# Optimization experiments

Measured on AMD Instinct MI355X. Metric: run time of the kernel, lower is better.

## Reference

```python
import jax, jax.numpy as jnp
import numpy as np

B, S, D, H, HS, OUT = 2, 2048, 1024, 16, 64, 1024
NEG = 1e12


def setup_inputs() -> dict:
    key = jax.random.key(0)
    ks = jax.random.split(key, 12)
    def glorot(k, shape):
        lim = np.sqrt(6.0 / (shape[0] + shape[1]))
        return jax.random.uniform(k, shape, jnp.float32, -lim, lim)
    return {
        'query': jax.random.normal(ks[0], (B, S, D), jnp.float32),
        'key':   jax.random.normal(ks[1], (B, S, D), jnp.float32),
        'value': jax.random.normal(ks[2], (B, S, D), jnp.float32),
        'Wq': glorot(ks[3], (D, H * HS)), 'bq': jnp.zeros((H * HS,), jnp.float32),
        'Wk': glorot(ks[4], (D, H * HS)), 'bk': jnp.zeros((H * HS,), jnp.float32),
        'Wv': glorot(ks[5], (D, H * HS)), 'bv': jnp.zeros((H * HS,), jnp.float32),
        'Wo': glorot(ks[6], (H * HS, OUT)), 'bo': jnp.zeros((OUT,), jnp.float32),
        'q_mask': jax.random.randint(ks[7], (B, S), 0, 2, jnp.int32),
        'v_mask': jax.random.randint(ks[8], (B, S), 0, 2, jnp.int32),
    }


def reference(query, key, value, Wq, bq, Wk, bk, Wv, bv, Wo, bo, q_mask, v_mask):
    qm = q_mask.astype(query.dtype)  # [B,Sq]
    vm = v_mask.astype(query.dtype)  # [B,Sk]
    # projections -> [B,S,H,HS]
    q = (query @ Wq + bq).reshape(B, S, H, HS)
    k = (key @ Wk + bk).reshape(B, S, H, HS)
    v = (value @ Wv + bv).reshape(B, S, H, HS)
    # scores [B,H,Sq,Sk]; code always divides by sqrt(head_size)
    a = jnp.einsum('bqhd,bkhd->bhqk', q, k) / np.sqrt(HS).astype(np.float32)
    a = a - (1.0 - vm[:, None, None, :]) * NEG  # additive padding mask on keys
    a = jax.nn.softmax(a, axis=-1)
    o = jnp.einsum('bhqk,bkhd->bqhd', a, v).reshape(B, S, H * HS)
    o = o @ Wo + bo
    o = o * qm[:, :, None]  # zero out padded query positions
    return o
```

## Files before the change

kernel.cpp:

```cpp
#include <hip/hip_runtime.h>

#define Bz 2
#define Sz 2048
#define Dz 1024
#define Hz 16
#define HSz 64
#define Mz 4096
#define NEGB (-1e30f)
#define CEXP 12.0f
#define QSCALE (0.125f * 1.44269504088896f)

typedef _Float16 f16;
typedef _Float16 f16x8 __attribute__((ext_vector_type(8)));
typedef _Float16 f16x4 __attribute__((ext_vector_type(4)));
typedef float f32x4 __attribute__((ext_vector_type(4)));

#define MFMA32(a, b, c) __builtin_amdgcn_mfma_f32_16x16x32_f16((a), (b), (c), 0, 0, 0)
#define MFMA16(a, b, c) __builtin_amdgcn_mfma_f32_16x16x16f16((a), (b), (c), 0, 0, 0)
#define EXP2(x) __builtin_amdgcn_exp2f(x)

__device__ __forceinline__ void gload16(const void* g, void* l) {
  __builtin_amdgcn_global_load_lds(
      (const __attribute__((address_space(1))) unsigned int*)(unsigned long long)g,
      (__attribute__((address_space(3))) unsigned int*)(unsigned int)(unsigned long long)l,
      16, 0, 0);
}
__device__ __forceinline__ void gload4(const void* g, void* l) {
  __builtin_amdgcn_global_load_lds(
      (const __attribute__((address_space(1))) unsigned int*)(unsigned long long)g,
      (__attribute__((address_space(3))) unsigned int*)(unsigned int)(unsigned long long)l,
      4, 0, 0);
}

__global__ __launch_bounds__(256) void k_prep(
    const float* __restrict__ q, const float* __restrict__ k,
    const float* __restrict__ v, f16* __restrict__ oq, f16* __restrict__ ok,
    f16* __restrict__ ov, const float* __restrict__ W0,
    const float* __restrict__ W1, const float* __restrict__ W2,
    const float* __restrict__ W3, f16* __restrict__ T0, f16* __restrict__ T1,
    f16* __restrict__ T2, f16* __restrict__ T3, const int* __restrict__ vm,
    float* __restrict__ vmb) {
  __shared__ float tbuf[32][33];
  const int bid = blockIdx.x;
  if (bid < 12288) {
    const int s = bid >> 12, cb = bid & 4095;
    const float* in = s == 0 ? q : s == 1 ? k : v;
    f16* out = s == 0 ? oq : s == 1 ? ok : ov;
    int i = (cb * 256 + threadIdx.x) * 4;
    f32x4 vv = *reinterpret_cast<const f32x4*>(in + i);
    f16x4 o;
    o[0] = (f16)vv[0]; o[1] = (f16)vv[1]; o[2] = (f16)vv[2]; o[3] = (f16)vv[3];
    *reinterpret_cast<f16x4*>(out + i) = o;
  } else if (bid < 16384) {
    const int r = bid - 12288;
    const int z = r >> 10, xy = r & 1023;
    const float* W = z == 0 ? W0 : z == 1 ? W1 : z == 2 ? W2 : W3;
    f16* T = z == 0 ? T0 : z == 1 ? T1 : z == 2 ? T2 : T3;
    const int tx = threadIdx.x & 31, ty = threadIdx.x >> 5;
    const int n0 = (xy & 31) * 32, k0 = (xy >> 5) * 32;
#pragma unroll
    for (int rr = 0; rr < 4; ++rr)
      tbuf[ty * 4 + rr][tx] = W[(size_t)(k0 + ty * 4 + rr) * Dz + n0 + tx];
    __syncthreads();
#pragma unroll
    for (int rr = 0; rr < 4; ++rr)
      T[(size_t)(n0 + ty * 4 + rr) * Dz + k0 + tx] = (f16)tbuf[tx][ty * 4 + rr];
  } else {
    int i = (bid - 16384) * 256 + threadIdx.x;
    vmb[i] = vm[i] ? -CEXP : NEGB;
  }
}

#define BMg 128
#define BNg 128
#define BKg 64
#define NKT (Dz / BKg)

#define GEMM_MAINLOOP(Aptr, Bptr)                                              \
  f32x4 acc[4][2] = {};                                                        \
  auto stage = [&](int kt, int buf) {                                          \
    const int k0 = kt * BKg;                                                   \
    _Pragma("unroll") for (int j = 0; j < 2; ++j) {                            \
      int c = j * 512 + t;                                                     \
      int row = c >> 3, p = c & 7;                                             \
      int ke = (p ^ (row & 7)) * 8;                                            \
      gload16(Aptr + (size_t)(m0 + row) * Dz + k0 + ke,                        \
              (char*)&As[buf][0] + c * 16);                                    \
      gload16(Bptr + (size_t)(n0 + row) * Dz + k0 + ke,                        \
              (char*)&Bs[buf][0] + c * 16);                                    \
    }                                                                          \
  };                                                                           \
  stage(0, 0);                                                                 \
  __syncthreads();                                                             \
  for (int kt = 0; kt < NKT; ++kt) {                                           \
    const int cur = kt & 1;                                                    \
    if (kt + 1 < NKT) stage(kt + 1, cur ^ 1);                                  \
    __builtin_amdgcn_s_setprio(1);                                             \
    _Pragma("unroll") for (int ks = 0; ks < 2; ++ks) {                         \
      f16x8 af[4], bf[2];                                                      \
      _Pragma("unroll") for (int fr = 0; fr < 4; ++fr) {                       \
        const int row = wr * 64 + fr * 16 + ll;                                \
        af[fr] = *reinterpret_cast<const f16x8*>(                              \
            &As[cur][row * 64 + (((ks * 4 + lh) ^ (row & 7)) * 8)]);           \
      }                                                                        \
      _Pragma("unroll") for (int fc = 0; fc < 2; ++fc) {                       \
        const int col = wc * 32 + fc * 16 + ll;                                \
        bf[fc] = *reinterpret_cast<const f16x8*>(                              \
            &Bs[cur][col * 64 + (((ks * 4 + lh) ^ (col & 7)) * 8)]);           \
      }                                                                        \
      _Pragma("unroll") for (int fr = 0; fr < 4; ++fr)                         \
          _Pragma("unroll") for (int fc = 0; fc < 2; ++fc)                     \
              acc[fr][fc] = MFMA32(af[fr], bf[fc], acc[fr][fc]);               \
    }                                                                          \
    __builtin_amdgcn_s_setprio(0);                                             \
    __syncthreads();                                                           \
  }

__global__ __launch_bounds__(512) void k_gemm_qkv(
    const f16* __restrict__ Xq, const f16* __restrict__ Xk,
    const f16* __restrict__ Xv, const f16* __restrict__ Wq,
    const f16* __restrict__ Wk, const f16* __restrict__ Wv,
    const float* __restrict__ bq, const float* __restrict__ bk,
    const float* __restrict__ bv, f16* __restrict__ Qh, f16* __restrict__ Kh,
    f16* __restrict__ Vth) {
  __shared__ f16 As[2][BMg * BKg];
  __shared__ f16 Bs[2][BNg * BKg];
  const int z = blockIdx.z;
  const f16* A = z == 0 ? Xq : z == 1 ? Xk : Xv;
  const f16* Bt = z == 0 ? Wq : z == 1 ? Wk : Wv;
  const float* bias = z == 0 ? bq : z == 1 ? bk : bv;
  f16* outh = z == 0 ? Qh : z == 1 ? Kh : Vth;
  const float oscale = z == 0 ? QSCALE : 1.0f;
  const int t = threadIdx.x, lane = t & 63, wv = t >> 6;
  const int ll = lane & 15, lh = lane >> 4;
  const int m0 = blockIdx.y * BMg, n0 = blockIdx.x * BNg;
  const int wr = wv >> 2, wc = wv & 3;

  GEMM_MAINLOOP(A, Bt)

#pragma unroll
  for (int fc = 0; fc < 2; ++fc) {
    const int n = n0 + wc * 32 + fc * 16 + ll;
    const float bn = bias[n];
#pragma unroll
    for (int fr = 0; fr < 4; ++fr)
#pragma unroll
      for (int i = 0; i < 4; ++i) {
        const int m = m0 + wr * 64 + fr * 16 + lh * 4 + i;
        float v = (acc[fr][fc][i] + bn) * oscale;
        if (z < 2) {
          outh[((size_t)((m >> 11) * Hz + (n >> 6))) * (Sz * HSz) +
               (size_t)(m & (Sz - 1)) * HSz + (n & 63)] = (f16)v;
        } else {
          outh[((size_t)((m >> 11) * Hz + (n >> 6))) * (HSz * Sz) +
               (size_t)(n & 63) * Sz + (m & (Sz - 1))] = (f16)v;
        }
      }
  }
}

__global__ __launch_bounds__(512) void k_gemm_o(
    const f16* __restrict__ A, const f16* __restrict__ Bt,
    const float* __restrict__ bias, float* __restrict__ outf,
    const int* __restrict__ qmask) {
  __shared__ f16 As[2][BMg * BKg];
  __shared__ f16 Bs[2][BNg * BKg];
  const int t = threadIdx.x, lane = t & 63, wv = t >> 6;
  const int ll = lane & 15, lh = lane >> 4;
  const int m0 = blockIdx.y * BMg, n0 = blockIdx.x * BNg;
  const int wr = wv >> 2, wc = wv & 3;

  GEMM_MAINLOOP(A, Bt)

#pragma unroll
  for (int fc = 0; fc < 2; ++fc) {
    const int n = n0 + wc * 32 + fc * 16 + ll;
    const float bn = bias[n];
#pragma unroll
    for (int fr = 0; fr < 4; ++fr)
#pragma unroll
      for (int i = 0; i < 4; ++i) {
        const int m = m0 + wr * 64 + fr * 16 + lh * 4 + i;
        outf[(size_t)m * Dz + n] = (acc[fr][fc][i] + bn) * (float)qmask[m];
      }
  }
}

#define QB 128
#define KBc 64
#define NST (Sz / (2 * KBc))

__global__ __launch_bounds__(256, 4) void k_attn(
    const f16* __restrict__ Q, const f16* __restrict__ K,
    const f16* __restrict__ Vt, const float* __restrict__ vmb,
    f16* __restrict__ attnA) {
  __shared__ f16 Kl[4][KBc * 64];
  __shared__ f16 Vl[4][HSz * 64];
  __shared__ float mbl[4][KBc];
  const int t = threadIdx.x, lane = t & 63, wv = t >> 6;
  const int ll = lane & 15, lh = lane >> 4;
  const int bh = blockIdx.y, b = bh >> 4, h = bh & 15;
  const int q0 = blockIdx.x * QB + wv * 32;
  const size_t base = (size_t)bh * Sz * HSz;

  f16x8 qf[2][2];
#pragma unroll
  for (int qs = 0; qs < 2; ++qs) {
    const f16* Qb = Q + base + (size_t)(q0 + qs * 16 + ll) * HSz;
    qf[qs][0] = *reinterpret_cast<const f16x8*>(&Qb[lh * 8]);
    qf[qs][1] = *reinterpret_cast<const f16x8*>(&Qb[32 + lh * 8]);
  }

  f32x4 acc0[4] = {}, acc1[4] = {};
  f32x4 accl0 = {}, accl1 = {};
  const f16x4 vone = {(f16)1.f, (f16)1.f, (f16)1.f, (f16)1.f};

  auto stage = [&](int key0, int pair) {
#pragma unroll
    for (int sb = 0; sb < 2; ++sb) {
      const int bi = pair * 2 + sb;
#pragma unroll
      for (int j = 0; j < 2; ++j) {
        int c = j * 256 + t;
        int r = c >> 3, p = c & 7, ps = (p ^ (r & 7)) * 8;
        gload16(K + base + (size_t)(key0 + sb * KBc + r) * HSz + ps,
                (char*)&Kl[bi][0] + c * 16);
        gload16(Vt + base + (size_t)r * Sz + key0 + sb * KBc + ps,
                (char*)&Vl[bi][0] + c * 16);
      }
      if (wv == 0)
        gload4(vmb + b * Sz + key0 + sb * KBc + lane,
               (char*)&mbl[bi][0] + lane * 4);
    }
  };

  auto tile = [&](int bi) {
    f32x4 sa0[4], sa1[4];
#pragma unroll
    for (int cf = 0; cf < 4; ++cf) {
      f32x4 mb = *reinterpret_cast<const f32x4*>(&mbl[bi][cf * 16 + lh * 4]);
      sa0[cf] = mb;
      sa1[cf] = mb;
    }
    __builtin_amdgcn_s_setprio(1);
#pragma unroll
    for (int cf = 0; cf < 4; ++cf) {
      const int row = cf * 16 + ll;
      const f16* kr = &Kl[bi][row * 64];
      f16x8 ka0 = *reinterpret_cast<const f16x8*>(&kr[(lh ^ (ll & 7)) * 8]);
      f16x8 ka1 = *reinterpret_cast<const f16x8*>(&kr[((4 + lh) ^ (ll & 7)) * 8]);
      sa0[cf] = MFMA32(ka0, qf[0][0], sa0[cf]);
      sa0[cf] = MFMA32(ka1, qf[0][1], sa0[cf]);
      sa1[cf] = MFMA32(ka0, qf[1][0], sa1[cf]);
      sa1[cf] = MFMA32(ka1, qf[1][1], sa1[cf]);
    }
    __builtin_amdgcn_s_setprio(0);

    f16x4 pb0[4], pb1[4];
#pragma unroll
    for (int cf = 0; cf < 4; ++cf) {
#pragma unroll
      for (int i = 0; i < 4; ++i) {
        pb0[cf][i] = (f16)EXP2(sa0[cf][i]);
        pb1[cf][i] = (f16)EXP2(sa1[cf][i]);
      }
    }

    __builtin_amdgcn_s_setprio(1);
#pragma unroll
    for (int hf = 0; hf < 4; ++hf) {
      const int row = hf * 16 + ll;
      const f16* vr = &Vl[bi][row * 64];
#pragma unroll
      for (int cf = 0; cf < 4; ++cf) {
        f16x4 va = *reinterpret_cast<const f16x4*>(
            &vr[((2 * cf + (lh >> 1)) ^ (ll & 7)) * 8 + (lh & 1) * 4]);
        acc0[hf] = MFMA16(va, pb0[cf], acc0[hf]);
        acc1[hf] = MFMA16(va, pb1[cf], acc1[hf]);
      }
    }
#pragma unroll
    for (int cf = 0; cf < 4; ++cf) {
      accl0 = MFMA16(vone, pb0[cf], accl0);
      accl1 = MFMA16(vone, pb1[cf], accl1);
    }
    __builtin_amdgcn_s_setprio(0);
  };

  stage(0, 0);
  __syncthreads();

  for (int st = 0; st < NST; ++st) {
    const int cur = st & 1;
    if (st + 1 < NST) stage((st + 1) * 2 * KBc, cur ^ 1);
    tile(cur * 2);
    tile(cur * 2 + 1);
    __syncthreads();
  }

#pragma unroll
  for (int qs = 0; qs < 2; ++qs) {
    const float l_run = qs ? accl1[0] : accl0[0];
    const float inv = 1.f / fmaxf(l_run, 1e-37f);
    const int q = q0 + qs * 16 + ll;
    f16* orow = attnA + (size_t)(b * Sz + q) * (Hz * HSz) + h * HSz;
#pragma unroll
    for (int hf = 0; hf < 4; ++hf) {
      const f32x4& a = qs ? acc1[hf] : acc0[hf];
      f16x4 ov;
#pragma unroll
      for (int i = 0; i < 4; ++i) ov[i] = (f16)(a[i] * inv);
      *reinterpret_cast<f16x4*>(&orow[hf * 16 + 4 * lh]) = ov;
    }
  }
}

extern "C" void kernel_launch(void* const* d_in, const int* in_sizes, int n_in,
                              void* d_out, int out_size, void* d_ws, size_t ws_size,
                              hipStream_t stream) {
  const float* query = (const float*)d_in[0];
  const float* key   = (const float*)d_in[1];
  const float* value = (const float*)d_in[2];
  const float* Wq = (const float*)d_in[3];
  const float* bq = (const float*)d_in[4];
  const float* Wk = (const float*)d_in[5];
  const float* bk = (const float*)d_in[6];
  const float* Wv = (const float*)d_in[7];
  const float* bv = (const float*)d_in[8];
  const float* Wo = (const float*)d_in[9];
  const float* bo = (const float*)d_in[10];
  const int* qm = (const int*)d_in[11];
  const int* vm = (const int*)d_in[12];

  f16* Xq  = (f16*)d_ws;
  f16* Xk  = Xq + 4194304;
  f16* Xv  = Xk + 4194304;
  f16* Wqh = Xv + 4194304;
  f16* Wkh = Wqh + 1048576;
  f16* Wvh = Wkh + 1048576;
  f16* Woh = Wvh + 1048576;
  f16* Qh  = Woh + 1048576;
  f16* Kh  = Qh + 4194304;
  f16* Vth = Kh + 4194304;
  f16* Ah  = Vth + 4194304;
  float* vmbias = (float*)(Ah + 4194304);

  k_prep<<<16400, 256, 0, stream>>>(query, key, value, Xq, Xk, Xv, Wq, Wk, Wv,
                                    Wo, Wqh, Wkh, Wvh, Woh, vm, vmbias);

  dim3 gq(Dz / BNg, Mz / BMg, 3);
  k_gemm_qkv<<<gq, 512, 0, stream>>>(Xq, Xk, Xv, Wqh, Wkh, Wvh, bq, bk, bv,
                                     Qh, Kh, Vth);

  dim3 ag(Sz / QB, Bz * Hz);
  k_attn<<<ag, 256, 0, stream>>>(Qh, Kh, Vth, vmbias, Ah);

  dim3 gg(Dz / BNg, Mz / BMg);
  k_gemm_o<<<gg, 512, 0, stream>>>(Ah, Woh, bo, (float*)d_out, qm);
}
```

Before: 130.9 us.

## Permute V-transpose key order for 16-byte LDS reads; shrink attention staging to 64-key tiles

The V projection epilogue now writes keys in a permuted order within each 64-key block, so the attention kernel can read V fragments as one 16-byte LDS load per pair of MFMA16 steps instead of two 8-byte loads. The permutation is consistent because P columns and V rows share the same permuted key order, and the sum over keys is unaffected. The attention loop is also restructured from 2×64-key stages over 4 LDS buffers to single 64-key tiles over 2 buffers. This halves LDS use, which could raise occupancy, but adds twice as many barriers per key sweep.

```diff
diff --git a/kernel.cpp b/kernel.cpp
--- a/kernel.cpp
+++ b/kernel.cpp
@@ -152,8 +152,9 @@
           outh[((size_t)((m >> 11) * Hz + (n >> 6))) * (Sz * HSz) +
                (size_t)(m & (Sz - 1)) * HSz + (n & 63)] = (f16)v;
         } else {
+          const int mp = (m & ~63) | (32 * (fr >> 1) + 8 * lh + 4 * (fr & 1) + i);
           outh[((size_t)((m >> 11) * Hz + (n >> 6))) * (HSz * Sz) +
-               (size_t)(n & 63) * Sz + (m & (Sz - 1))] = (f16)v;
+               (size_t)(n & 63) * Sz + (mp & (Sz - 1))] = (f16)v;
         }
       }
   }
@@ -188,15 +189,15 @@
 
 #define QB 128
 #define KBc 64
-#define NST (Sz / (2 * KBc))
+#define NT (Sz / KBc)
 
 __global__ __launch_bounds__(256, 4) void k_attn(
     const f16* __restrict__ Q, const f16* __restrict__ K,
     const f16* __restrict__ Vt, const float* __restrict__ vmb,
     f16* __restrict__ attnA) {
-  __shared__ f16 Kl[4][KBc * 64];
-  __shared__ f16 Vl[4][HSz * 64];
-  __shared__ float mbl[4][KBc];
+  __shared__ f16 Kl[2][KBc * 64];
+  __shared__ f16 Vl[2][HSz * 64];
+  __shared__ float mbl[2][KBc];
   const int t = threadIdx.x, lane = t & 63, wv = t >> 6;
   const int ll = lane & 15, lh = lane >> 4;
   const int bh = blockIdx.y, b = bh >> 4, h = bh & 15;
@@ -215,30 +216,29 @@
   f32x4 accl0 = {}, accl1 = {};
   const f16x4 vone = {(f16)1.f, (f16)1.f, (f16)1.f, (f16)1.f};
 
-  auto stage = [&](int key0, int pair) {
-#pragma unroll
-    for (int sb = 0; sb < 2; ++sb) {
-      const int bi = pair * 2 + sb;
-#pragma unroll
-      for (int j = 0; j < 2; ++j) {
-        int c = j * 256 + t;
-        int r = c >> 3, p = c & 7, ps = (p ^ (r & 7)) * 8;
-        gload16(K + base + (size_t)(key0 + sb * KBc + r) * HSz + ps,
-                (char*)&Kl[bi][0] + c * 16);
-        gload16(Vt + base + (size_t)r * Sz + key0 + sb * KBc + ps,
-                (char*)&Vl[bi][0] + c * 16);
-      }
-      if (wv == 0)
-        gload4(vmb + b * Sz + key0 + sb * KBc + lane,
-               (char*)&mbl[bi][0] + lane * 4);
-    }
+  auto stage = [&](int key0, int buf) {
+#pragma unroll
+    for (int j = 0; j < 2; ++j) {
+      int c = j * 256 + t;
+      int r = c >> 3, p = c & 7, ps = (p ^ (r & 7)) * 8;
+      gload16(K + base + (size_t)(key0 + r) * HSz + ps, (char*)&Kl[buf][0] + c * 16);
+      gload16(Vt + base + (size_t)r * Sz + key0 + ps, (char*)&Vl[buf][0] + c * 16);
+    }
+    if (wv == 0)
+      gload4(vmb + b * Sz + key0 + lane, (char*)&mbl[buf][0] + lane * 4);
   };
 
-  auto tile = [&](int bi) {
+  stage(0, 0);
+  __syncthreads();
+
+  for (int kt = 0; kt < NT; ++kt) {
+    const int cur = kt & 1;
+    if (kt + 1 < NT) stage((kt + 1) * KBc, cur ^ 1);
+
     f32x4 sa0[4], sa1[4];
 #pragma unroll
     for (int cf = 0; cf < 4; ++cf) {
-      f32x4 mb = *reinterpret_cast<const f32x4*>(&mbl[bi][cf * 16 + lh * 4]);
+      f32x4 mb = *reinterpret_cast<const f32x4*>(&mbl[cur][cf * 16 + lh * 4]);
       sa0[cf] = mb;
       sa1[cf] = mb;
     }
@@ -246,7 +246,7 @@
 #pragma unroll
     for (int cf = 0; cf < 4; ++cf) {
       const int row = cf * 16 + ll;
-      const f16* kr = &Kl[bi][row * 64];
+      const f16* kr = &Kl[cur][row * 64];
       f16x8 ka0 = *reinterpret_cast<const f16x8*>(&kr[(lh ^ (ll & 7)) * 8]);
       f16x8 ka1 = *reinterpret_cast<const f16x8*>(&kr[((4 + lh) ^ (ll & 7)) * 8]);
       sa0[cf] = MFMA32(ka0, qf[0][0], sa0[cf]);
@@ -270,13 +270,17 @@
 #pragma unroll
     for (int hf = 0; hf < 4; ++hf) {
       const int row = hf * 16 + ll;
-      const f16* vr = &Vl[bi][row * 64];
-#pragma unroll
-      for (int cf = 0; cf < 4; ++cf) {
-        f16x4 va = *reinterpret_cast<const f16x4*>(
-            &vr[((2 * cf + (lh >> 1)) ^ (ll & 7)) * 8 + (lh & 1) * 4]);
-        acc0[hf] = MFMA16(va, pb0[cf], acc0[hf]);
-        acc1[hf] = MFMA16(va, pb1[cf], acc1[hf]);
+      const f16* vr = &Vl[cur][row * 64];
+#pragma unroll
+      for (int P = 0; P < 2; ++P) {
+        f16x8 v8 = *reinterpret_cast<const f16x8*>(
+            &vr[((4 * P + lh) ^ (ll & 7)) * 8]);
+        f16x4 vlo = {v8[0], v8[1], v8[2], v8[3]};
+        f16x4 vhi = {v8[4], v8[5], v8[6], v8[7]};
+        acc0[hf] = MFMA16(vlo, pb0[2 * P], acc0[hf]);
+        acc1[hf] = MFMA16(vlo, pb1[2 * P], acc1[hf]);
+        acc0[hf] = MFMA16(vhi, pb0[2 * P + 1], acc0[hf]);
+        acc1[hf] = MFMA16(vhi, pb1[2 * P + 1], acc1[hf]);
       }
     }
 #pragma unroll
@@ -285,16 +289,6 @@
       accl1 = MFMA16(vone, pb1[cf], accl1);
     }
     __builtin_amdgcn_s_setprio(0);
-  };
-
-  stage(0, 0);
-  __syncthreads();
-
-  for (int st = 0; st < NST; ++st) {
-    const int cur = st & 1;
-    if (st + 1 < NST) stage((st + 1) * 2 * KBc, cur ^ 1);
-    tile(cur * 2);
-    tile(cur * 2 + 1);
     __syncthreads();
   }
 
```

Measured after the change: 128.4 us. No clear change (-1.9%).
